# Optimization experiments

Measured on AMD Instinct MI355X. Metric: run time of the kernel, lower is better.

Reference implementation:

```python
import jax, jax.numpy as jnp
import numpy as np
import math

D_MODEL = 1024
N_HEADS = 16
D_K = D_MODEL // N_HEADS
BSZ = 4
SEQ = 2048


def setup_inputs() -> dict:
    key = jax.random.key(0)
    ks = jax.random.split(key, 10)
    x = jax.random.normal(ks[0], (BSZ, SEQ, D_MODEL), dtype=jnp.float32)
    pad_mask = jnp.zeros((BSZ, 1, 1, SEQ), dtype=jnp.int32)
    s = 0.02
    Wq = jax.random.normal(ks[1], (D_MODEL, D_MODEL), jnp.float32) * s
    bq = jax.random.normal(ks[2], (D_MODEL,), jnp.float32) * s
    Wk = jax.random.normal(ks[3], (D_MODEL, D_MODEL), jnp.float32) * s
    bk = jax.random.normal(ks[4], (D_MODEL,), jnp.float32) * s
    Wv = jax.random.normal(ks[5], (D_MODEL, D_MODEL), jnp.float32) * s
    bv = jax.random.normal(ks[6], (D_MODEL,), jnp.float32) * s
    Wo = jax.random.normal(ks[7], (D_MODEL, D_MODEL), jnp.float32) * s
    bo = jax.random.normal(ks[8], (D_MODEL,), jnp.float32) * s
    return {"x": x, "pad_mask": pad_mask, "Wq": Wq, "bq": bq, "Wk": Wk,
            "bk": bk, "Wv": Wv, "bv": bv, "Wo": Wo, "bo": bo}


def reference(x, pad_mask, Wq, bq, Wk, bk, Wv, bv, Wo, bo):
    bsz, seq_len, d_model = x.shape
    h, dk = N_HEADS, D_K

    def split(W, b):
        # torch Linear: x @ W.T + b ; then [b,s,h,dk] -> [b,h,s,dk]
        y = jnp.einsum('bsd,ed->bse', x, W) + b
        return y.reshape(bsz, seq_len, h, dk).transpose(0, 2, 1, 3)

    q = split(Wq, bq)
    k = split(Wk, bk)
    v = split(Wv, bv)

    scores = jnp.einsum('bhqd,bhkd->bhqk', q, k) / math.sqrt(dk)
    causal = jnp.triu(jnp.ones((seq_len, seq_len), dtype=bool), k=1)
    scores = jnp.where(causal[None, None], -jnp.inf, scores)
    scores = jnp.where(pad_mask == 1, -jnp.inf, scores)
    attn = jax.nn.softmax(scores, axis=-1)
    attn = jnp.nan_to_num(attn, nan=0.0)
    out = jnp.einsum('bhqk,bhkd->bhqd', attn, v)
    out = out.transpose(0, 2, 1, 3).reshape(bsz, seq_len, d_model)
    # dropout is identity in eval mode
    return jnp.einsum('bsd,ed->bse', out, Wo) + bo
```

## Files before the change

### kernel.cpp

```cpp
#include <hip/hip_runtime.h>
#include <stdint.h>
#include <stddef.h>


typedef __bf16 bf16;
typedef __bf16 bf16x8 __attribute__((ext_vector_type(8)));
typedef __bf16 bf16x4 __attribute__((ext_vector_type(4)));
typedef float f32x4 __attribute__((ext_vector_type(4)));

#define DM   1024
#define NH   16
#define DK   64
#define BSZ  4
#define SEQL 2048
#define NTOK 8192
#define NEGB -3.0e38f

__device__ __forceinline__ void async16(const bf16* g, bf16* l) {
  __builtin_amdgcn_global_load_lds(
      (__attribute__((address_space(1))) void*)g,
      (__attribute__((address_space(3))) void*)l, 16, 0, 0);
}

__global__ __launch_bounds__(256) void cvt_all(
    const float* __restrict__ x,
    const float* __restrict__ w0, const float* __restrict__ w1,
    const float* __restrict__ w2, const float* __restrict__ w3,
    const int* __restrict__ pad,
    bf16* __restrict__ xd,
    bf16* __restrict__ d0, bf16* __restrict__ d1,
    bf16* __restrict__ d2, bf16* __restrict__ d3,
    float* __restrict__ padf) {
  int blk = blockIdx.x;
  if (blk >= 6144) {
    int i = (blk - 6144) * 2048 + threadIdx.x * 8;
    int4 p0 = *(const int4*)(pad + i);
    int4 p1 = *(const int4*)(pad + i + 4);
    float4 o0 = {p0.x ? NEGB : 0.f, p0.y ? NEGB : 0.f, p0.z ? NEGB : 0.f, p0.w ? NEGB : 0.f};
    float4 o1 = {p1.x ? NEGB : 0.f, p1.y ? NEGB : 0.f, p1.z ? NEGB : 0.f, p1.w ? NEGB : 0.f};
    *(float4*)(padf + i) = o0;
    *(float4*)(padf + i + 4) = o1;
    return;
  }
  const float* s; bf16* d; int i;
  if (blk < 4096) { s = x; d = xd; i = blk * 2048 + threadIdx.x * 8; }
  else {
    int m = (blk - 4096) >> 9, bi = (blk - 4096) & 511;
    switch (m) {
      case 0:  s = w0; d = d0; break;
      case 1:  s = w1; d = d1; break;
      case 2:  s = w2; d = d2; break;
      default: s = w3; d = d3; break;
    }
    i = bi * 2048 + threadIdx.x * 8;
  }
  float4 v0 = *(const float4*)(s + i);
  float4 v1 = *(const float4*)(s + i + 4);
  bf16x8 o = {(bf16)v0.x, (bf16)v0.y, (bf16)v0.z, (bf16)v0.w,
              (bf16)v1.x, (bf16)v1.y, (bf16)v1.z, (bf16)v1.w};
  *(bf16x8*)(d + i) = o;
}

template <int OUT_MODE>
__device__ __forceinline__ void gemm128(const bf16* __restrict__ A,
                                        const bf16* __restrict__ W,
                                        const float* __restrict__ bias,
                                        void* __restrict__ outp) {
  __shared__ bf16 As[128 * 32];
  __shared__ bf16 Bs[128 * 32];
  const int tid  = threadIdx.x;
  const int lane = tid & 63;
  const int wv   = tid >> 6;
  const int wm   = (wv & 1) * 64;
  const int wn   = (wv >> 1) * 64;
  const int c    = lane & 15;
  const int quad = lane >> 4;
  const int bm   = blockIdx.y * 128;
  const int bn   = blockIdx.x * 128;

  f32x4 acc[4][4] = {};

  for (int k0 = 0; k0 < DM; k0 += 32) {
    __syncthreads();
#pragma unroll
    for (int j = 0; j < 2; ++j) {
      int i = j * 256 + tid;
      async16(A + (size_t)(bm + (i >> 2)) * DM + k0 + (i & 3) * 8, As + i * 8);
      async16(W + (size_t)(bn + (i >> 2)) * DM + k0 + (i & 3) * 8, Bs + i * 8);
    }
    __syncthreads();
    bf16x8 af[4], bg[4];
#pragma unroll
    for (int mi = 0; mi < 4; ++mi)
      af[mi] = *(const bf16x8*)&As[(wm + mi * 16 + c) * 32 + quad * 8];
#pragma unroll
    for (int ni = 0; ni < 4; ++ni)
      bg[ni] = *(const bf16x8*)&Bs[(wn + ni * 16 + c) * 32 + quad * 8];
#pragma unroll
    for (int mi = 0; mi < 4; ++mi)
#pragma unroll
      for (int ni = 0; ni < 4; ++ni)
        acc[mi][ni] = __builtin_amdgcn_mfma_f32_16x16x32_bf16(af[mi], bg[ni],
                                                              acc[mi][ni], 0, 0, 0);
  }

  float bias_r[4];
#pragma unroll
  for (int ni = 0; ni < 4; ++ni) bias_r[ni] = bias[bn + wn + ni * 16 + c];

  if constexpr (OUT_MODE == 2) {
    __shared__ bf16 Vtr[4][64 * 72];
    bf16* vt = &Vtr[wv][0];
#pragma unroll
    for (int mi = 0; mi < 4; ++mi)
#pragma unroll
      for (int ni = 0; ni < 4; ++ni) {
        bf16x4 pv = {(bf16)(acc[mi][ni][0] + bias_r[ni]),
                     (bf16)(acc[mi][ni][1] + bias_r[ni]),
                     (bf16)(acc[mi][ni][2] + bias_r[ni]),
                     (bf16)(acc[mi][ni][3] + bias_r[ni])};
        *(bf16x4*)&vt[(ni * 16 + c) * 72 + mi * 16 + quad * 4] = pv;
      }
    const int base = bm + wm;
    const int bb = base >> 11, s0 = base & 2047;
    const int rl = lane >> 3, cl = lane & 7;
#pragma unroll
    for (int it = 0; it < 8; ++it) {
      int d_row = it * 8 + rl;
      bf16x8 v = *(const bf16x8*)&vt[d_row * 72 + cl * 8];
      int n_g = bn + wn + d_row;
      int hh = n_g >> 6, dd = n_g & 63;
      *(bf16x8*)&((bf16*)outp)[(((size_t)(bb * NH + hh)) * DK + dd) * SEQL + s0 + cl * 8] = v;
    }
    return;
  }

#pragma unroll
  for (int mi = 0; mi < 4; ++mi) {
#pragma unroll
    for (int reg = 0; reg < 4; ++reg) {
      int m_g = bm + wm + mi * 16 + quad * 4 + reg;
#pragma unroll
      for (int ni = 0; ni < 4; ++ni) {
        int n_g = bn + wn + ni * 16 + c;
        float v = acc[mi][ni][reg] + bias_r[ni];
        if (OUT_MODE == 0) {
          int b = m_g >> 11, s = m_g & 2047;
          int h = n_g >> 6, d = n_g & 63;
          ((bf16*)outp)[(((size_t)(b * NH + h) * SEQL + s) << 6) + d] = (bf16)v;
        } else {
          ((float*)outp)[(size_t)m_g * DM + n_g] = v;
        }
      }
    }
  }
}

__global__ __launch_bounds__(256) void qkv_gemm(
    const bf16* __restrict__ X,
    const bf16* __restrict__ Wq, const bf16* __restrict__ Wk, const bf16* __restrict__ Wv,
    const float* __restrict__ bq, const float* __restrict__ bk, const float* __restrict__ bv,
    bf16* __restrict__ Q, bf16* __restrict__ K, bf16* __restrict__ Vt) {
  if (blockIdx.z == 0)      gemm128<0>(X, Wq, bq, Q);
  else if (blockIdx.z == 1) gemm128<0>(X, Wk, bk, K);
  else                      gemm128<2>(X, Wv, bv, Vt);
}

__global__ __launch_bounds__(256) void out_gemm(const bf16* __restrict__ A,
                                                const bf16* __restrict__ W,
                                                const float* __restrict__ bias,
                                                float* __restrict__ out) {
  gemm128<1>(A, W, bias, out);
}

#define PSTR 40

__global__ __launch_bounds__(512) void attn_kernel(
    const bf16* __restrict__ Q, const bf16* __restrict__ K,
    const bf16* __restrict__ Vt, const float* __restrict__ padf,
    bf16* __restrict__ O) {
  const int B = blockIdx.x;
  const int xcd = B & 7;
  const int g = B >> 3;
  const int bh = xcd + 8 * (g >> 3);
  const int t = g & 7;
  const int b = bh >> 4, h = bh & 15;
  const int tid  = threadIdx.x;
  const int lane = tid & 63;
  const int wv   = tid >> 6;
  const int c    = lane & 15;
  const int quad = lane >> 4;

  __shared__ bf16 KsS[2][32 * 64];
  __shared__ bf16 VsS[2][64 * 32];
  __shared__ bf16 Plds_all[8][16 * PSTR];
  bf16* Plds = &Plds_all[wv][0];

  const bf16* Qh  = Q  + (size_t)bh * SEQL * DK;
  const bf16* Kh  = K  + (size_t)bh * SEQL * DK;
  const bf16* Vth = Vt + (size_t)bh * DK * SEQL;
  const float* pb = padf + b * SEQL;

  const bool stK = (wv < 4);
  const int kr = lane >> 3;
  const int kj = (lane & 7) ^ kr;
  const int vr = lane >> 2;
  const int vj = (lane & 3) ^ (vr & 3);
  const size_t sgoff = stK ? (size_t)(wv * 8 + kr) * DK + kj * 8
                           : (size_t)((wv - 4) * 16 + vr) * SEQL + vj * 8;
  const bf16* sgbase = stK ? Kh : Vth;
  bf16* sl0 = stK ? &KsS[0][(wv * 64 + lane) * 8] : &VsS[0][((wv - 4) * 64 + lane) * 8];
  bf16* sl1 = stK ? &KsS[1][(wv * 64 + lane) * 8] : &VsS[1][((wv - 4) * 64 + lane) * 8];
  const size_t sstep = stK ? (size_t)32 * DK : 32;

  const float sc = 0.1803368801111204f;

  for (int pass = 0; pass < 2; ++pass) {
    const int qt  = pass ? 15 - t : t;
    const int R   = qt * 128 + wv * 16;
    const int nkt = (qt + 1) * 4;

    bf16x8 Qf[2];
#pragma unroll
    for (int kh = 0; kh < 2; ++kh)
      Qf[kh] = *(const bf16x8*)&Qh[(size_t)(R + c) * DK + kh * 32 + quad * 8];

    f32x4 Oc[4] = {};
    float l_s = 0.f;

    __syncthreads();
    async16(sgbase + sgoff, sl0);

    for (int kt = 0; kt < nkt; ++kt) {
      const int cur = kt & 1;
      const int kb = kt * 32;
      __syncthreads();

      if (kt + 1 < nkt)
        async16(sgbase + (size_t)(kt + 1) * sstep + sgoff, (cur ? sl0 : sl1));
      if (kb > R + 15) continue;

      float4 bc[2];
#pragma unroll
      for (int kf = 0; kf < 2; ++kf)
        bc[kf] = *(const float4*)&pb[kb + kf * 16 + quad * 4];

      bf16x8 Kf[2][2], Vf[4];
#pragma unroll
      for (int kf = 0; kf < 2; ++kf) {
        const int rloc = kf * 16 + c;
#pragma unroll
        for (int kh = 0; kh < 2; ++kh) {
          const int j = kh * 4 + quad;
          Kf[kf][kh] = *(const bf16x8*)&KsS[cur][(rloc * 8 + (j ^ (rloc & 7))) * 8];
        }
      }
#pragma unroll
      for (int df = 0; df < 4; ++df) {
        const int dloc = df * 16 + c;
        Vf[df] = *(const bf16x8*)&VsS[cur][(dloc * 4 + (quad ^ (dloc & 3))) * 8];
      }

      f32x4 st[2] = {};
#pragma unroll
      for (int kh = 0; kh < 2; ++kh)
#pragma unroll
        for (int kf = 0; kf < 2; ++kf)
          st[kf] = __builtin_amdgcn_mfma_f32_16x16x32_bf16(Kf[kf][kh], Qf[kh],
                                                           st[kf], 0, 0, 0);

      const bool diag = (kb + 31 > R);
      float p8[8];
#pragma unroll
      for (int kf = 0; kf < 2; ++kf) {
        const float* bv4 = (const float*)&bc[kf];
#pragma unroll
        for (int r = 0; r < 4; ++r) {
          float e = __builtin_amdgcn_exp2f(__builtin_fmaf(st[kf][r], sc, bv4[r]));
          if (diag && (kb + kf * 16 + quad * 4 + r > R + c)) e = 0.f;
          p8[kf * 4 + r] = e;
          l_s += e;
        }
      }
      bf16x4 pk0 = {(bf16)p8[0], (bf16)p8[1], (bf16)p8[2], (bf16)p8[3]};
      bf16x4 pk1 = {(bf16)p8[4], (bf16)p8[5], (bf16)p8[6], (bf16)p8[7]};
      *(bf16x4*)&Plds[c * PSTR + quad * 4] = pk0;
      *(bf16x4*)&Plds[c * PSTR + 16 + quad * 4] = pk1;

      bf16x8 af = *(const bf16x8*)&Plds[c * PSTR + quad * 8];
#pragma unroll
      for (int df = 0; df < 4; ++df)
        Oc[df] = __builtin_amdgcn_mfma_f32_16x16x32_bf16(af, Vf[df], Oc[df], 0, 0, 0);
    }

    float l = l_s;
    l += __shfl_xor(l, 16);
    l += __shfl_xor(l, 32);
    float linv = (l > 0.f) ? 1.f / l : 0.f;
    float lr[4];
#pragma unroll
    for (int r = 0; r < 4; ++r) lr[r] = __shfl(linv, quad * 4 + r);
#pragma unroll
    for (int r = 0; r < 4; ++r) {
      size_t row = (size_t)(b * SEQL + R + quad * 4 + r) * DM + h * DK;
#pragma unroll
      for (int df = 0; df < 4; ++df)
        O[row + df * 16 + c] = (bf16)(Oc[df][r] * lr[r]);
    }
  }
}

extern "C" void kernel_launch(void* const* d_in, const int* in_sizes, int n_in,
                              void* d_out, int out_size, void* d_ws, size_t ws_size,
                              hipStream_t stream) {
  const float* x   = (const float*)d_in[0];
  const int*   pad = (const int*)d_in[1];
  const float* Wq  = (const float*)d_in[2];
  const float* bq  = (const float*)d_in[3];
  const float* Wk  = (const float*)d_in[4];
  const float* bk  = (const float*)d_in[5];
  const float* Wv  = (const float*)d_in[6];
  const float* bv  = (const float*)d_in[7];
  const float* Wo  = (const float*)d_in[8];
  const float* bo  = (const float*)d_in[9];
  float* out = (float*)d_out;

  const size_t SZ_X = (size_t)NTOK * DM * 2;
  const size_t SZ_W = (size_t)DM * DM * 2;
  char* ws = (char*)d_ws;
  bf16* Xb  = (bf16*)ws;  ws += SZ_X;
  bf16* Wqb = (bf16*)ws;  ws += SZ_W;
  bf16* Wkb = (bf16*)ws;  ws += SZ_W;
  bf16* Wvb = (bf16*)ws;  ws += SZ_W;
  bf16* Wob = (bf16*)ws;  ws += SZ_W;
  bf16* Qb  = (bf16*)ws;  ws += SZ_X;
  bf16* Kb  = (bf16*)ws;  ws += SZ_X;
  bf16* Vtb = (bf16*)ws;  ws += SZ_X;
  bf16* Ob  = (bf16*)ws;  ws += SZ_X;
  float* padfb = (float*)ws; ws += (size_t)NTOK * 4;

  cvt_all<<<6148, 256, 0, stream>>>(x, Wq, Wk, Wv, Wo, pad,
                                    Xb, Wqb, Wkb, Wvb, Wob, padfb);
  qkv_gemm<<<dim3(8, 64, 3), 256, 0, stream>>>(Xb, Wqb, Wkb, Wvb, bq, bk, bv, Qb, Kb, Vtb);
  attn_kernel<<<512, 512, 0, stream>>>(Qb, Kb, Vtb, padfb, Ob);
  out_gemm<<<dim3(8, 64), 256, 0, stream>>>(Ob, Wob, bo, out);
}
```

Measured before the change: 274.0 us.

## Rewrite projection GEMMs with 128x256 tiles, triple-buffered async LDS pipeline, swizzle

```diff
diff --git a/kernel.cpp b/kernel.cpp
--- a/kernel.cpp
+++ b/kernel.cpp
@@ -16,7 +16,7 @@
 #define NTOK 8192
 #define NEGB -3.0e38f
 
-__device__ __forceinline__ void async16(const bf16* g, bf16* l) {
+__device__ __forceinline__ void async16(const bf16* g, void* l) {
   __builtin_amdgcn_global_load_lds(
       (__attribute__((address_space(1))) void*)g,
       (__attribute__((address_space(3))) void*)l, 16, 0, 0);
@@ -62,55 +62,105 @@
 }
 
 template <int OUT_MODE>
-__device__ __forceinline__ void gemm128(const bf16* __restrict__ A,
-                                        const bf16* __restrict__ W,
-                                        const float* __restrict__ bias,
-                                        void* __restrict__ outp) {
-  __shared__ bf16 As[128 * 32];
-  __shared__ bf16 Bs[128 * 32];
+__device__ __forceinline__ void gemm_core(const bf16* __restrict__ A,
+                                          const bf16* __restrict__ W,
+                                          const float* __restrict__ bias,
+                                          void* __restrict__ outp,
+                                          int bm, int bn, char* smem) {
   const int tid  = threadIdx.x;
   const int lane = tid & 63;
   const int wv   = tid >> 6;
-  const int wm   = (wv & 1) * 64;
-  const int wn   = (wv >> 1) * 64;
+  const int wr   = wv >> 2;
+  const int wc   = wv & 3;
   const int c    = lane & 15;
   const int quad = lane >> 4;
-  const int bm   = blockIdx.y * 128;
-  const int bn   = blockIdx.x * 128;
+
+  const int sr = tid >> 3;
+  const int sj = ((tid & 7) ^ (sr & 7)) << 3;
+  const bf16* gA = A + (size_t)(bm + sr) * DM + sj;
+  const bf16* gB = W + (size_t)(bn + sr) * DM + sj;
+
+#define STAGE_A(TT, TGT) {                                        \
+    char* la_ = smem + (TGT) * 49152 + tid * 16;                  \
+    async16(gA + (size_t)(TT) * 64, la_);                         \
+    async16(gA + (size_t)64 * DM + (size_t)(TT) * 64, la_ + 8192); }
+#define STAGE_B(TT, TGT) {                                        \
+    char* lb_ = smem + (TGT) * 49152 + 16384 + tid * 16;          \
+    async16(gB + (size_t)(TT) * 64, lb_);                         \
+    async16(gB + (size_t)64 * DM + (size_t)(TT) * 64, lb_ + 8192);  \
+    async16(gB + (size_t)128 * DM + (size_t)(TT) * 64, lb_ + 16384); \
+    async16(gB + (size_t)192 * DM + (size_t)(TT) * 64, lb_ + 24576); }
+
+  int aoff[2][4], boff[2][4];
+#pragma unroll
+  for (int kk = 0; kk < 2; ++kk) {
+    const int sw = ((kk * 4 + quad) ^ (c & 7)) << 4;
+#pragma unroll
+    for (int i = 0; i < 4; ++i) {
+      aoff[kk][i] = (wr * 64 + i * 16 + c) * 128 + sw;
+      boff[kk][i] = 16384 + (wc * 64 + i * 16 + c) * 128 + sw;
+    }
+  }
 
   f32x4 acc[4][4] = {};
 
-  for (int k0 = 0; k0 < DM; k0 += 32) {
+  STAGE_A(0, 0) STAGE_B(0, 0)
+  STAGE_A(1, 1) STAGE_B(1, 1)
+  asm volatile("s_waitcnt vmcnt(6)" ::: "memory");
+  __builtin_amdgcn_s_barrier();
+  __builtin_amdgcn_sched_barrier(0);
+
+#pragma unroll
+  for (int T = 0; T < 16; ++T) {
+    const char* bufc = smem + (T % 3) * 49152;
+    const int TGT = (T + 2) % 3;
+    bf16x8 a0[4], b0[4], a1[4], b1[4];
+#pragma unroll
+    for (int i = 0; i < 4; ++i) a0[i] = *(const bf16x8*)(bufc + aoff[0][i]);
+#pragma unroll
+    for (int i = 0; i < 4; ++i) b0[i] = *(const bf16x8*)(bufc + boff[0][i]);
+    __builtin_amdgcn_sched_barrier(0);
+#pragma unroll
+    for (int i = 0; i < 4; ++i) a1[i] = *(const bf16x8*)(bufc + aoff[1][i]);
+#pragma unroll
+    for (int i = 0; i < 4; ++i) b1[i] = *(const bf16x8*)(bufc + boff[1][i]);
+    if (T < 14) { STAGE_A(T + 2, TGT) STAGE_B(T + 2, TGT) }
+    __builtin_amdgcn_s_barrier();
+    asm volatile("s_waitcnt lgkmcnt(8)" ::: "memory");
+    __builtin_amdgcn_sched_barrier(0);
+    __builtin_amdgcn_s_setprio(1);
+#pragma unroll
+    for (int mi = 0; mi < 4; ++mi)
+#pragma unroll
+      for (int ni = 0; ni < 4; ++ni)
+        acc[mi][ni] = __builtin_amdgcn_mfma_f32_16x16x32_bf16(a0[mi], b0[ni],
+                                                              acc[mi][ni], 0, 0, 0);
+    __builtin_amdgcn_s_setprio(0);
+    asm volatile("s_waitcnt lgkmcnt(0)" ::: "memory");
+    __builtin_amdgcn_sched_barrier(0);
+    __builtin_amdgcn_s_setprio(1);
+#pragma unroll
+    for (int mi = 0; mi < 4; ++mi)
+#pragma unroll
+      for (int ni = 0; ni < 4; ++ni)
+        acc[mi][ni] = __builtin_amdgcn_mfma_f32_16x16x32_bf16(a1[mi], b1[ni],
+                                                              acc[mi][ni], 0, 0, 0);
+    __builtin_amdgcn_s_setprio(0);
+    if (T < 14)       asm volatile("s_waitcnt vmcnt(6)" ::: "memory");
+    else if (T == 14) asm volatile("s_waitcnt vmcnt(0)" ::: "memory");
+    __builtin_amdgcn_s_barrier();
+    __builtin_amdgcn_sched_barrier(0);
+  }
+#undef STAGE_A
+#undef STAGE_B
+
+  float bias_r[4];
+#pragma unroll
+  for (int ni = 0; ni < 4; ++ni) bias_r[ni] = bias[bn + wc * 64 + ni * 16 + c];
+
+  if constexpr (OUT_MODE == 2) {
     __syncthreads();
-#pragma unroll
-    for (int j = 0; j < 2; ++j) {
-      int i = j * 256 + tid;
-      async16(A + (size_t)(bm + (i >> 2)) * DM + k0 + (i & 3) * 8, As + i * 8);
-      async16(W + (size_t)(bn + (i >> 2)) * DM + k0 + (i & 3) * 8, Bs + i * 8);
-    }
-    __syncthreads();
-    bf16x8 af[4], bg[4];
-#pragma unroll
-    for (int mi = 0; mi < 4; ++mi)
-      af[mi] = *(const bf16x8*)&As[(wm + mi * 16 + c) * 32 + quad * 8];
-#pragma unroll
-    for (int ni = 0; ni < 4; ++ni)
-      bg[ni] = *(const bf16x8*)&Bs[(wn + ni * 16 + c) * 32 + quad * 8];
-#pragma unroll
-    for (int mi = 0; mi < 4; ++mi)
-#pragma unroll
-      for (int ni = 0; ni < 4; ++ni)
-        acc[mi][ni] = __builtin_amdgcn_mfma_f32_16x16x32_bf16(af[mi], bg[ni],
-                                                              acc[mi][ni], 0, 0, 0);
-  }
-
-  float bias_r[4];
-#pragma unroll
-  for (int ni = 0; ni < 4; ++ni) bias_r[ni] = bias[bn + wn + ni * 16 + c];
-
-  if constexpr (OUT_MODE == 2) {
-    __shared__ bf16 Vtr[4][64 * 72];
-    bf16* vt = &Vtr[wv][0];
+    bf16* vt = (bf16*)smem + wv * 4608;
 #pragma unroll
     for (int mi = 0; mi < 4; ++mi)
 #pragma unroll
@@ -121,14 +171,14 @@
                      (bf16)(acc[mi][ni][3] + bias_r[ni])};
         *(bf16x4*)&vt[(ni * 16 + c) * 72 + mi * 16 + quad * 4] = pv;
       }
-    const int base = bm + wm;
+    const int base = bm + wr * 64;
     const int bb = base >> 11, s0 = base & 2047;
     const int rl = lane >> 3, cl = lane & 7;
 #pragma unroll
     for (int it = 0; it < 8; ++it) {
       int d_row = it * 8 + rl;
       bf16x8 v = *(const bf16x8*)&vt[d_row * 72 + cl * 8];
-      int n_g = bn + wn + d_row;
+      int n_g = bn + wc * 64 + d_row;
       int hh = n_g >> 6, dd = n_g & 63;
       *(bf16x8*)&((bf16*)outp)[(((size_t)(bb * NH + hh)) * DK + dd) * SEQL + s0 + cl * 8] = v;
     }
@@ -139,10 +189,10 @@
   for (int mi = 0; mi < 4; ++mi) {
 #pragma unroll
     for (int reg = 0; reg < 4; ++reg) {
-      int m_g = bm + wm + mi * 16 + quad * 4 + reg;
+      int m_g = bm + wr * 64 + mi * 16 + quad * 4 + reg;
 #pragma unroll
       for (int ni = 0; ni < 4; ++ni) {
-        int n_g = bn + wn + ni * 16 + c;
+        int n_g = bn + wc * 64 + ni * 16 + c;
         float v = acc[mi][ni][reg] + bias_r[ni];
         if (OUT_MODE == 0) {
           int b = m_g >> 11, s = m_g & 2047;
@@ -156,21 +206,31 @@
   }
 }
 
-__global__ __launch_bounds__(256) void qkv_gemm(
+__global__ __launch_bounds__(512, 2) void qkv_gemm(
     const bf16* __restrict__ X,
     const bf16* __restrict__ Wq, const bf16* __restrict__ Wk, const bf16* __restrict__ Wv,
     const float* __restrict__ bq, const float* __restrict__ bk, const float* __restrict__ bv,
     bf16* __restrict__ Q, bf16* __restrict__ K, bf16* __restrict__ Vt) {
-  if (blockIdx.z == 0)      gemm128<0>(X, Wq, bq, Q);
-  else if (blockIdx.z == 1) gemm128<0>(X, Wk, bk, K);
-  else                      gemm128<2>(X, Wv, bv, Vt);
-}
-
-__global__ __launch_bounds__(256) void out_gemm(const bf16* __restrict__ A,
-                                                const bf16* __restrict__ W,
-                                                const float* __restrict__ bias,
-                                                float* __restrict__ out) {
-  gemm128<1>(A, W, bias, out);
+  __shared__ alignas(16) char smem[147456];
+  const int f = blockIdx.x;
+  const int wg = (f & 7) * 96 + (f >> 3);
+  const int y = wg / 12, t = wg % 12;
+  const int z = t >> 2, x = t & 3;
+  const int bm = y * 128, bn = x * 256;
+  if (z < 2)
+    gemm_core<0>(X, z ? Wk : Wq, z ? bk : bq, z ? (void*)K : (void*)Q, bm, bn, smem);
+  else
+    gemm_core<2>(X, Wv, bv, Vt, bm, bn, smem);
+}
+
+__global__ __launch_bounds__(512, 2) void out_gemm(const bf16* __restrict__ A,
+                                                   const bf16* __restrict__ W,
+                                                   const float* __restrict__ bias,
+                                                   float* __restrict__ out) {
+  __shared__ alignas(16) char smem[147456];
+  const int f = blockIdx.x;
+  const int wg = (f & 7) * 32 + (f >> 3);
+  gemm_core<1>(A, W, bias, out, (wg >> 2) * 128, (wg & 3) * 256, smem);
 }
 
 #define PSTR 40
@@ -341,7 +401,7 @@
 
   cvt_all<<<6148, 256, 0, stream>>>(x, Wq, Wk, Wv, Wo, pad,
                                     Xb, Wqb, Wkb, Wvb, Wob, padfb);
-  qkv_gemm<<<dim3(8, 64, 3), 256, 0, stream>>>(Xb, Wqb, Wkb, Wvb, bq, bk, bv, Qb, Kb, Vtb);
+  qkv_gemm<<<768, 512, 0, stream>>>(Xb, Wqb, Wkb, Wvb, bq, bk, bv, Qb, Kb, Vtb);
   attn_kernel<<<512, 512, 0, stream>>>(Qb, Kb, Vtb, padfb, Ob);
-  out_gemm<<<dim3(8, 64), 256, 0, stream>>>(Ob, Wob, bo, out);
-}
+  out_gemm<<<256, 512, 0, stream>>>(Ob, Wob, bo, out);
+}
```

Result: faster. 244.7 us (-10.7%).
